# Kernel optimization log

Hardware: AMD Instinct MI355X
Metric: run time of the kernel (lower is better)

Reference implementation:

```python
import jax, jax.numpy as jnp
import numpy as np

N = 100000   # nodes
E = 500000   # edges (expander + local)
DIM = 256    # dim_h
H = 8        # num_heads
DH = DIM // H
EPS_Z = 1e-6
EPS_BN = 1e-5


def setup_inputs() -> dict:
    key = jax.random.key(0)
    ks = jax.random.split(key, 8)
    s = 1.0 / np.sqrt(DIM).astype(np.float32)
    x = jax.random.normal(ks[0], (N, DIM), jnp.float32)
    edge_index = jax.random.randint(ks[1], (2, E), 0, N, dtype=jnp.int64)
    edge_attr = jax.random.normal(ks[2], (E, DIM), jnp.float32)
    WQ = jax.random.normal(ks[3], (DIM, DIM), jnp.float32) * s
    WK = jax.random.normal(ks[4], (DIM, DIM), jnp.float32) * s
    WE = jax.random.normal(ks[5], (DIM, DIM), jnp.float32) * s
    WV = jax.random.normal(ks[6], (DIM, DIM), jnp.float32) * s
    gamma = jnp.ones((DIM,), jnp.float32)
    beta = jnp.zeros((DIM,), jnp.float32)
    return dict(x=x, edge_attr=edge_attr, WQ=WQ, WK=WK, WE=WE, WV=WV,
                gamma=gamma, beta=beta, edge_index=edge_index)


def reference(x, edge_attr, WQ, WK, WE, WV, gamma, beta, edge_index):
    src, dst = edge_index[0], edge_index[1]
    # Linear projections (no bias), split into heads: [N, H, DH]
    Q = (x @ WQ).reshape(N, H, DH)
    K = (x @ WK).reshape(N, H, DH)
    V = (x @ WV).reshape(N, H, DH)
    Eh = (edge_attr @ WE).reshape(E, H, DH)
    scale = np.float32(1.0 / np.sqrt(DH))
    # Per-edge attention score: elementwise K_src * Q_dst * E, summed over DH
    score = K[src] * Q[dst] * scale * Eh                 # [E, H, DH]
    score = jnp.exp(jnp.clip(score.sum(-1, keepdims=True), -5.0, 5.0))  # [E, H, 1]
    msg = V[src] * score                                 # [E, H, DH]
    wV = jax.ops.segment_sum(msg, dst, num_segments=N)   # [N, H, DH]
    Z = jax.ops.segment_sum(score, dst, num_segments=N)  # [N, H, 1]
    h_attn = (wV / (Z + EPS_Z)).reshape(N, DIM)
    # dropout p=0 -> identity; residual add
    h = x + h_attn
    # BatchNorm1d, training mode (batch stats, biased variance)
    mean = h.mean(axis=0)
    var = ((h - mean) ** 2).mean(axis=0)
    return (h - mean) * jax.lax.rsqrt(var + EPS_BN) * gamma + beta
```

## Files before the change

### kernel.cpp

```cpp
#include <hip/hip_runtime.h>
#include <hip/hip_bf16.h>

#define N_NODES 100000
#define N_EDGES 500000
#define DIM 256
#define NH 8
#define DH 32

typedef short short8 __attribute__((ext_vector_type(8)));
typedef float f32x4 __attribute__((ext_vector_type(4)));

__device__ __forceinline__ unsigned short f2bf(float f) {
    unsigned u = __float_as_uint(f);
    unsigned r = (u + 0x7FFFu + ((u >> 16) & 1u)) >> 16;
    return (unsigned short)r;
}
__device__ __forceinline__ float bf2f(unsigned short u) {
    return __uint_as_float(((unsigned)u) << 16);
}

__global__ __launch_bounds__(256) void wconvert(const float* __restrict__ W,
                                                unsigned short* __restrict__ WT) {
    int t = blockIdx.x * 256 + threadIdx.x;
    int n = t >> 8, k = t & 255;
    WT[n * 256 + k] = f2bf(W[k * 256 + n]);
}

__global__ __launch_bounds__(256) void gemm_bf16(const float* __restrict__ A,
                                                 const unsigned short* __restrict__ WT,
                                                 unsigned short* __restrict__ C, int M) {
    __shared__ unsigned short Blds[256 * 32];
    const int tid = threadIdx.x;
    const int wave = tid >> 6, lane = tid & 63;
    const int quad = lane >> 4, col = lane & 15;
    const int base = blockIdx.x * 64 + wave * 16;
    const int arow = min(base + col, M - 1);

    f32x4 acc[16];
#pragma unroll
    for (int i = 0; i < 16; i++) acc[i] = (f32x4){0.f, 0.f, 0.f, 0.f};

    for (int kc = 0; kc < 8; kc++) {
        __syncthreads();
#pragma unroll
        for (int it = 0; it < 4; it++) {
            int e = it * 2048 + tid * 8;
            int n = e >> 5, j = e & 31;
            *(short8*)(&Blds[n * 32 + j]) = *(const short8*)(&WT[n * 256 + kc * 32 + j]);
        }
        __syncthreads();
        const float* ap = A + (long)arow * 256 + kc * 32 + quad * 8;
        float4 a0 = *(const float4*)ap;
        float4 a1 = *(const float4*)(ap + 4);
        short8 af;
        af[0] = f2bf(a0.x); af[1] = f2bf(a0.y); af[2] = f2bf(a0.z); af[3] = f2bf(a0.w);
        af[4] = f2bf(a1.x); af[5] = f2bf(a1.y); af[6] = f2bf(a1.z); af[7] = f2bf(a1.w);
#pragma unroll
        for (int nt = 0; nt < 16; nt++) {
            short8 bf = *(const short8*)(&Blds[(nt * 16 + col) * 32 + quad * 8]);
            acc[nt] = __builtin_amdgcn_mfma_f32_16x16x32_bf16(af, bf, acc[nt], 0, 0, 0);
        }
    }
#pragma unroll
    for (int nt = 0; nt < 16; nt++) {
#pragma unroll
        for (int r = 0; r < 4; r++) {
            int orow = base + quad * 4 + r;
            if (orow < M) C[(long)orow * 256 + nt * 16 + col] = f2bf(acc[nt][r]);
        }
    }
}

__global__ __launch_bounds__(256) void hist_kernel(const int* __restrict__ ei,
                                                   int* __restrict__ counts) {
    int e = blockIdx.x * 256 + threadIdx.x;
    if (e < N_EDGES) atomicAdd(&counts[ei[N_EDGES + e]], 1);
}

__global__ __launch_bounds__(1024) void scan_kernel(const int* __restrict__ counts,
                                                    int* __restrict__ offs,
                                                    int* __restrict__ cursor) {
    __shared__ int tsum[1024];
    const int t = threadIdx.x;
    const int CH = (N_NODES + 1023) / 1024;
    int lo = t * CH;
    int hi = min(lo + CH, N_NODES);
    int s = 0;
    for (int i = lo; i < hi; i++) s += counts[i];
    tsum[t] = s;
    __syncthreads();
    for (int d = 1; d < 1024; d <<= 1) {
        int v = (t >= d) ? tsum[t - d] : 0;
        __syncthreads();
        tsum[t] += v;
        __syncthreads();
    }
    int run = (t == 0) ? 0 : tsum[t - 1];
    for (int i = lo; i < hi; i++) {
        offs[i] = run;
        cursor[i] = run;
        run += counts[i];
    }
    if (t == 1023) offs[N_NODES] = run;
}

__global__ __launch_bounds__(256) void scatter_kernel(const int* __restrict__ ei,
                                                      int* __restrict__ cursor,
                                                      int2* __restrict__ epair) {
    int e = blockIdx.x * 256 + threadIdx.x;
    if (e >= N_EDGES) return;
    int dst = ei[N_EDGES + e];
    int pos = atomicAdd(&cursor[dst], 1);
    epair[pos] = make_int2(e, ei[e]);
}

__global__ __launch_bounds__(256) void node_kernel(const unsigned short* __restrict__ Qb,
                                                   const unsigned short* __restrict__ Kb,
                                                   const unsigned short* __restrict__ Vb,
                                                   const unsigned short* __restrict__ Ehb,
                                                   const float* __restrict__ x,
                                                   const int* __restrict__ offs,
                                                   const int2* __restrict__ epair,
                                                   float* __restrict__ h,
                                                   float* __restrict__ csum,
                                                   float* __restrict__ csumsq) {
    __shared__ float lsum[256], lss[256];
    const int wave = threadIdx.x >> 6, lane = threadIdx.x & 63;
    lsum[threadIdx.x] = 0.f;
    lss[threadIdx.x] = 0.f;
    __syncthreads();

    float s0 = 0.f, s1 = 0.f, s2 = 0.f, s3 = 0.f;
    float q0 = 0.f, q1 = 0.f, q2 = 0.f, q3 = 0.f;

    for (int n = blockIdx.x * 4 + wave; n < N_NODES; n += gridDim.x * 4) {
        ushort4 qv = ((const ushort4*)(Qb + (long)n * 256))[lane];
        float qx = bf2f(qv.x), qy = bf2f(qv.y), qz = bf2f(qv.z), qw = bf2f(qv.w);
        f32x4 acc = (f32x4){0.f, 0.f, 0.f, 0.f};
        float zh = 0.f;
        const int beg = offs[n], end = offs[n + 1];
        for (int idx = beg; idx < end; idx++) {
            int2 p = epair[idx];
            const long eoff = (long)p.x * 256;
            const long soff = (long)p.y * 256;
            ushort4 k4 = ((const ushort4*)(Kb + soff))[lane];
            ushort4 e4 = ((const ushort4*)(Ehb + eoff))[lane];
            ushort4 v4 = ((const ushort4*)(Vb + soff))[lane];
            float s = bf2f(k4.x) * qx * bf2f(e4.x)
                    + bf2f(k4.y) * qy * bf2f(e4.y)
                    + bf2f(k4.z) * qz * bf2f(e4.z)
                    + bf2f(k4.w) * qw * bf2f(e4.w);
            s += __shfl_xor(s, 1);
            s += __shfl_xor(s, 2);
            s += __shfl_xor(s, 4);
            s *= 0.17677669529663687f;
            s = fminf(fmaxf(s, -5.f), 5.f);
            float sc = __expf(s);
            acc[0] += bf2f(v4.x) * sc;
            acc[1] += bf2f(v4.y) * sc;
            acc[2] += bf2f(v4.z) * sc;
            acc[3] += bf2f(v4.w) * sc;
            zh += sc;
        }
        float inv = 1.f / (zh + 1e-6f);
        float4 xv = *(const float4*)(x + (long)n * 256 + lane * 4);
        float o0 = xv.x + acc[0] * inv;
        float o1 = xv.y + acc[1] * inv;
        float o2 = xv.z + acc[2] * inv;
        float o3 = xv.w + acc[3] * inv;
        float4 ov = {o0, o1, o2, o3};
        *(float4*)(h + (long)n * 256 + lane * 4) = ov;
        s0 += o0; s1 += o1; s2 += o2; s3 += o3;
        q0 += o0 * o0; q1 += o1 * o1; q2 += o2 * o2; q3 += o3 * o3;
    }

    int c = lane * 4;
    atomicAdd(&lsum[c + 0], s0); atomicAdd(&lss[c + 0], q0);
    atomicAdd(&lsum[c + 1], s1); atomicAdd(&lss[c + 1], q1);
    atomicAdd(&lsum[c + 2], s2); atomicAdd(&lss[c + 2], q2);
    atomicAdd(&lsum[c + 3], s3); atomicAdd(&lss[c + 3], q3);
    __syncthreads();
    atomicAdd(&csum[threadIdx.x], lsum[threadIdx.x]);
    atomicAdd(&csumsq[threadIdx.x], lss[threadIdx.x]);
}

__global__ __launch_bounds__(256) void bn_pass2(float* __restrict__ h,
                                                const float* __restrict__ csum,
                                                const float* __restrict__ csumsq,
                                                const float* __restrict__ gamma,
                                                const float* __restrict__ beta) {
    const float invN = 1.0f / N_NODES;
    const long total = (long)N_NODES * 256;
    for (long i = (long)blockIdx.x * 256 + threadIdx.x; i < total; i += (long)gridDim.x * 256) {
        int c = (int)(i & 255);
        float mean = csum[c] * invN;
        float var = csumsq[c] * invN - mean * mean;
        h[i] = (h[i] - mean) * rsqrtf(var + 1e-5f) * gamma[c] + beta[c];
    }
}

extern "C" void kernel_launch(void* const* d_in, const int* in_sizes, int n_in,
                              void* d_out, int out_size, void* d_ws, size_t ws_size,
                              hipStream_t stream) {
    const float* x     = (const float*)d_in[0];
    const float* ea    = (const float*)d_in[1];
    const float* WQ    = (const float*)d_in[2];
    const float* WK    = (const float*)d_in[3];
    const float* WE    = (const float*)d_in[4];
    const float* WV    = (const float*)d_in[5];
    const float* gamma = (const float*)d_in[6];
    const float* beta  = (const float*)d_in[7];
    const int*   ei    = (const int*)d_in[8];
    float* out = (float*)d_out;

    char* ws = (char*)d_ws;
    size_t off = 0;
    auto alloc = [&](size_t bytes) -> void* {
        void* p = ws + off;
        off = (off + bytes + 255) & ~(size_t)255;
        return p;
    };
    unsigned short* WTq = (unsigned short*)alloc(65536 * 2);
    unsigned short* WTk = (unsigned short*)alloc(65536 * 2);
    unsigned short* WTe = (unsigned short*)alloc(65536 * 2);
    unsigned short* WTv = (unsigned short*)alloc(65536 * 2);
    unsigned short* Qb  = (unsigned short*)alloc((size_t)N_NODES * 256 * 2);
    unsigned short* Kb  = (unsigned short*)alloc((size_t)N_NODES * 256 * 2);
    unsigned short* Vb  = (unsigned short*)alloc((size_t)N_NODES * 256 * 2);
    unsigned short* Ehb = (unsigned short*)alloc((size_t)N_EDGES * 256 * 2);
    int*   counts = (int*)alloc((size_t)N_NODES * 4);
    float* csum   = (float*)alloc(256 * 4);
    float* csumsq = (float*)alloc(256 * 4);
    char*  zend   = ws + off;
    int*   offs   = (int*)alloc((size_t)(N_NODES + 1) * 4);
    int*   cursor = (int*)alloc((size_t)N_NODES * 4);
    int2*  epair  = (int2*)alloc((size_t)N_EDGES * 8);

    wconvert<<<256, 256, 0, stream>>>(WQ, WTq);
    wconvert<<<256, 256, 0, stream>>>(WK, WTk);
    wconvert<<<256, 256, 0, stream>>>(WE, WTe);
    wconvert<<<256, 256, 0, stream>>>(WV, WTv);

    hipMemsetAsync(counts, 0, (size_t)(zend - (char*)counts), stream);

    hist_kernel<<<(N_EDGES + 255) / 256, 256, 0, stream>>>(ei, counts);
    scan_kernel<<<1, 1024, 0, stream>>>(counts, offs, cursor);
    scatter_kernel<<<(N_EDGES + 255) / 256, 256, 0, stream>>>(ei, cursor, epair);

    gemm_bf16<<<(N_NODES + 63) / 64, 256, 0, stream>>>(x, WTq, Qb, N_NODES);
    gemm_bf16<<<(N_NODES + 63) / 64, 256, 0, stream>>>(x, WTk, Kb, N_NODES);
    gemm_bf16<<<(N_NODES + 63) / 64, 256, 0, stream>>>(x, WTv, Vb, N_NODES);
    gemm_bf16<<<(N_EDGES + 63) / 64, 256, 0, stream>>>(ea, WTe, Ehb, N_EDGES);

    node_kernel<<<2048, 256, 0, stream>>>(Qb, Kb, Vb, Ehb, x, offs, epair,
                                          out, csum, csumsq);

    bn_pass2<<<4096, 256, 0, stream>>>(out, csum, csumsq, gamma, beta);
}
```

Before: 1.482 ms.

## Split edge score computation into a separate per-edge kernel before aggregation

Measured after the change: 1.586 ms. +7.0%, slower.

```diff
diff --git a/kernel.cpp b/kernel.cpp
--- a/kernel.cpp
+++ b/kernel.cpp
@@ -114,10 +114,33 @@
     epair[pos] = make_int2(e, ei[e]);
 }
 
-__global__ __launch_bounds__(256) void node_kernel(const unsigned short* __restrict__ Qb,
-                                                   const unsigned short* __restrict__ Kb,
-                                                   const unsigned short* __restrict__ Vb,
-                                                   const unsigned short* __restrict__ Ehb,
+__global__ __launch_bounds__(256) void score_kernel(const unsigned short* __restrict__ Qb,
+                                                    const unsigned short* __restrict__ Kb,
+                                                    const unsigned short* __restrict__ Ehb,
+                                                    const int* __restrict__ ei,
+                                                    float* __restrict__ score) {
+    const int wave = threadIdx.x >> 6, lane = threadIdx.x & 63;
+    const int e = blockIdx.x * 4 + wave;
+    const int src = ei[e];
+    const int dst = ei[N_EDGES + e];
+    ushort4 k4 = ((const ushort4*)(Kb + (long)src * 256))[lane];
+    ushort4 q4 = ((const ushort4*)(Qb + (long)dst * 256))[lane];
+    ushort4 e4 = ((const ushort4*)(Ehb + (long)e * 256))[lane];
+    float s = bf2f(k4.x) * bf2f(q4.x) * bf2f(e4.x)
+            + bf2f(k4.y) * bf2f(q4.y) * bf2f(e4.y)
+            + bf2f(k4.z) * bf2f(q4.z) * bf2f(e4.z)
+            + bf2f(k4.w) * bf2f(q4.w) * bf2f(e4.w);
+    s += __shfl_xor(s, 1);
+    s += __shfl_xor(s, 2);
+    s += __shfl_xor(s, 4);
+    s *= 0.17677669529663687f;
+    s = fminf(fmaxf(s, -5.f), 5.f);
+    float sc = __expf(s);
+    if ((lane & 7) == 0) score[(long)e * 8 + (lane >> 3)] = sc;
+}
+
+__global__ __launch_bounds__(256) void node_kernel(const unsigned short* __restrict__ Vb,
+                                                   const float* __restrict__ score,
                                                    const float* __restrict__ x,
                                                    const int* __restrict__ offs,
                                                    const int2* __restrict__ epair,
@@ -126,6 +149,7 @@
                                                    float* __restrict__ csumsq) {
     __shared__ float lsum[256], lss[256];
     const int wave = threadIdx.x >> 6, lane = threadIdx.x & 63;
+    const int head = lane >> 3;
     lsum[threadIdx.x] = 0.f;
     lss[threadIdx.x] = 0.f;
     __syncthreads();
@@ -134,28 +158,13 @@
     float q0 = 0.f, q1 = 0.f, q2 = 0.f, q3 = 0.f;
 
     for (int n = blockIdx.x * 4 + wave; n < N_NODES; n += gridDim.x * 4) {
-        ushort4 qv = ((const ushort4*)(Qb + (long)n * 256))[lane];
-        float qx = bf2f(qv.x), qy = bf2f(qv.y), qz = bf2f(qv.z), qw = bf2f(qv.w);
         f32x4 acc = (f32x4){0.f, 0.f, 0.f, 0.f};
         float zh = 0.f;
         const int beg = offs[n], end = offs[n + 1];
         for (int idx = beg; idx < end; idx++) {
             int2 p = epair[idx];
-            const long eoff = (long)p.x * 256;
-            const long soff = (long)p.y * 256;
-            ushort4 k4 = ((const ushort4*)(Kb + soff))[lane];
-            ushort4 e4 = ((const ushort4*)(Ehb + eoff))[lane];
-            ushort4 v4 = ((const ushort4*)(Vb + soff))[lane];
-            float s = bf2f(k4.x) * qx * bf2f(e4.x)
-                    + bf2f(k4.y) * qy * bf2f(e4.y)
-                    + bf2f(k4.z) * qz * bf2f(e4.z)
-                    + bf2f(k4.w) * qw * bf2f(e4.w);
-            s += __shfl_xor(s, 1);
-            s += __shfl_xor(s, 2);
-            s += __shfl_xor(s, 4);
-            s *= 0.17677669529663687f;
-            s = fminf(fmaxf(s, -5.f), 5.f);
-            float sc = __expf(s);
+            float sc = score[(long)p.x * 8 + head];
+            ushort4 v4 = ((const ushort4*)(Vb + (long)p.y * 256))[lane];
             acc[0] += bf2f(v4.x) * sc;
             acc[1] += bf2f(v4.y) * sc;
             acc[2] += bf2f(v4.z) * sc;
@@ -235,6 +244,7 @@
     int*   offs   = (int*)alloc((size_t)(N_NODES + 1) * 4);
     int*   cursor = (int*)alloc((size_t)N_NODES * 4);
     int2*  epair  = (int2*)alloc((size_t)N_EDGES * 8);
+    float* scores = (float*)alloc((size_t)N_EDGES * 8 * 4);
 
     wconvert<<<256, 256, 0, stream>>>(WQ, WTq);
     wconvert<<<256, 256, 0, stream>>>(WK, WTk);
@@ -252,7 +262,9 @@
     gemm_bf16<<<(N_NODES + 63) / 64, 256, 0, stream>>>(x, WTv, Vb, N_NODES);
     gemm_bf16<<<(N_EDGES + 63) / 64, 256, 0, stream>>>(ea, WTe, Ehb, N_EDGES);
 
-    node_kernel<<<2048, 256, 0, stream>>>(Qb, Kb, Vb, Ehb, x, offs, epair,
+    score_kernel<<<N_EDGES / 4, 256, 0, stream>>>(Qb, Kb, Ehb, ei, scores);
+
+    node_kernel<<<4096, 256, 0, stream>>>(Vb, scores, x, offs, epair,
                                           out, csum, csumsq);
 
     bn_pass2<<<4096, 256, 0, stream>>>(out, csum, csumsq, gamma, beta);
```
